# Kernel tuning notes

Hardware: AMD Instinct MI355X
Metric: run time of the kernel (lower is better)

The kernel has to match this reference:

```python
import jax, jax.numpy as jnp
import numpy as np

MIN_S = 0.05
MAX_S = 0.3
B, D = 16384, 2048
H = D // 4


def setup_inputs() -> dict:
    key = jax.random.key(0)
    k1, k2, k3 = jax.random.split(key, 3)
    x = jax.random.normal(k1, (B, D), dtype=jnp.float32)
    # sparsity predictor params (stored [in, out]); torch Linear default init scale
    s1 = 1.0 / np.sqrt(D)
    s2 = 1.0 / np.sqrt(H)
    W1 = jax.random.uniform(k2, (D, H), jnp.float32, -s1, s1)
    b1 = jnp.zeros((H,), jnp.float32)
    W2 = jax.random.uniform(k3, (H, 1), jnp.float32, -s2, s2)
    b2 = jnp.zeros((1,), jnp.float32)
    return {"x": x, "W1": W1, "b1": b1, "W2": W2, "b2": b2}


def reference(x, W1, b1, W2, b2):
    # sparsity predictor: Linear -> ReLU -> Linear -> Sigmoid, scaled to [min,max]
    h = jax.nn.relu(x @ W1 + b1)                         # [B, H]
    sig = jax.nn.sigmoid(h @ W2 + b2)                    # [B, 1]
    sparsity = MIN_S + (MAX_S - MIN_S) * sig             # [B, 1]

    d = x.shape[1]
    abs_x = jnp.abs(x)
    # per-row k = max(1, round(D * (1 - s))); torch uses Python round (half-even),
    # matching jnp.round semantics
    k = jnp.maximum(1, jnp.round(d * (1.0 - sparsity[:, 0])).astype(jnp.int32))  # [B]
    sorted_abs = jnp.sort(abs_x, axis=1)                 # [B, D] ascending
    threshold = jnp.take_along_axis(sorted_abs, (k - 1)[:, None], axis=1)        # [B, 1]

    mask = (abs_x > threshold).astype(x.dtype)           # [B, D]
    sparse_x = x * mask
    actual_sparsity = mask.sum(axis=1) / d               # [B]
    l1_reg = jnp.abs(sparse_x).sum(axis=1).mean()        # scalar
    return sparse_x, mask, sparsity, actual_sparsity, l1_reg
```

## Files before the change

kernel.cpp:

```cpp
#include <hip/hip_runtime.h>
#include <math.h>

#define B_ROWS 16384
#define D_DIM  2048
#define H_DIM  512

typedef __attribute__((ext_vector_type(8))) short  s16x8;
typedef __attribute__((ext_vector_type(4))) float  f32x4;

union U8 { unsigned short us[8]; s16x8 v; };
union U4 { unsigned short us[4]; short4 v; };

static __device__ __forceinline__ unsigned short f2bf(float f) {
    unsigned u = __float_as_uint(f);
    u += 0x7FFFu + ((u >> 16) & 1u);
    return (unsigned short)(u >> 16);
}

__global__ __launch_bounds__(256) void pack_w1(
    const float* __restrict__ W1, unsigned short* __restrict__ Wp)
{
    const int gid = blockIdx.x * 256 + threadIdx.x;
    const int ko = gid >> 9;
    const int n  = gid & 511;
    U8 h8, l8;
    #pragma unroll
    for (int j = 0; j < 8; ++j) {
        const float w = W1[(size_t)(ko * 8 + j) * H_DIM + n];
        const unsigned short h = f2bf(w);
        const float hf = __uint_as_float((unsigned)h << 16);
        h8.us[j] = h;
        l8.us[j] = f2bf(w - hf);
    }
    const int s    = ko >> 2;
    const int lane = (n & 15) | ((ko & 3) << 4);
    const int Nt   = n >> 4;
    const size_t baseH = ((((size_t)0 * 64 + s) * 32 + Nt) * 64 + lane) * 8;
    const size_t baseL = ((((size_t)1 * 64 + s) * 32 + Nt) * 64 + lane) * 8;
    *(s16x8*)(Wp + baseH) = h8.v;
    *(s16x8*)(Wp + baseL) = l8.v;
}

__global__ __launch_bounds__(512, 2) void predictor_gemm(
    const float* __restrict__ x, const unsigned short* __restrict__ Wp,
    const float* __restrict__ b1, const float* __restrict__ W2,
    double* __restrict__ logit)
{
    __shared__ __align__(16) unsigned short Abuf[2][2][2048];

    const int tid = threadIdx.x;
    const int l   = tid & 63;
    const int Nw  = tid >> 6;
    const int bx  = blockIdx.x;
    const int rowBase = bx * 64;
    const int NtBase  = Nw * 4;

    const int sm = tid >> 3;
    const int sh = tid & 7;
    const float* xp = x + (size_t)(rowBase + sm) * D_DIM + sh * 4;
    const int stIdx = (sm >> 4) * 512 + (((sm & 15) | ((sh >> 1) << 4)) << 3) + (sh & 1) * 4;
    unsigned short* stH[2] = {&Abuf[0][0][stIdx], &Abuf[1][0][stIdx]};
    unsigned short* stL[2] = {&Abuf[0][1][stIdx], &Abuf[1][1][stIdx]};

    const s16x8* WpV = (const s16x8*)Wp;

    f32x4 acc[4][4];
    #pragma unroll
    for (int mt = 0; mt < 4; ++mt)
        #pragma unroll
        for (int nt = 0; nt < 4; ++nt)
            acc[mt][nt] = {0.f, 0.f, 0.f, 0.f};

    {
        const float4 v = *(const float4*)(xp);
        const float xv[4] = {v.x, v.y, v.z, v.w};
        U4 h4, l4;
        #pragma unroll
        for (int j = 0; j < 4; ++j) {
            const unsigned short h = f2bf(xv[j]);
            h4.us[j] = h;
            l4.us[j] = f2bf(xv[j] - __uint_as_float((unsigned)h << 16));
        }
        *(short4*)stH[0] = h4.v;
        *(short4*)stL[0] = l4.v;
    }
    s16x8 Bh[4], Bl[4];
    #pragma unroll
    for (int nt = 0; nt < 4; ++nt) {
        Bh[nt] = WpV[((0 * 64 + 0) * 32 + NtBase + nt) * 64 + l];
        Bl[nt] = WpV[((1 * 64 + 0) * 32 + NtBase + nt) * 64 + l];
    }
    __syncthreads();

    for (int s = 0; s < 64; ++s) {
        const int cur = s & 1, nxt = cur ^ 1;
        s16x8 BhN[4], BlN[4];
        float4 xn;
        if (s < 63) {
            #pragma unroll
            for (int nt = 0; nt < 4; ++nt) {
                BhN[nt] = WpV[((0 * 64 + (s + 1)) * 32 + NtBase + nt) * 64 + l];
                BlN[nt] = WpV[((1 * 64 + (s + 1)) * 32 + NtBase + nt) * 64 + l];
            }
            xn = *(const float4*)(xp + (s + 1) * 32);
        }

        s16x8 Ah[4], Al[4];
        #pragma unroll
        for (int mt = 0; mt < 4; ++mt) {
            Ah[mt] = *(const s16x8*)&Abuf[cur][0][mt * 512 + l * 8];
            Al[mt] = *(const s16x8*)&Abuf[cur][1][mt * 512 + l * 8];
        }

        #pragma unroll
        for (int mt = 0; mt < 4; ++mt)
            #pragma unroll
            for (int nt = 0; nt < 4; ++nt) {
                acc[mt][nt] = __builtin_amdgcn_mfma_f32_16x16x32_bf16(Ah[mt], Bh[nt], acc[mt][nt], 0, 0, 0);
                acc[mt][nt] = __builtin_amdgcn_mfma_f32_16x16x32_bf16(Al[mt], Bh[nt], acc[mt][nt], 0, 0, 0);
                acc[mt][nt] = __builtin_amdgcn_mfma_f32_16x16x32_bf16(Ah[mt], Bl[nt], acc[mt][nt], 0, 0, 0);
            }

        if (s < 63) {
            const float xv[4] = {xn.x, xn.y, xn.z, xn.w};
            U4 h4, l4;
            #pragma unroll
            for (int j = 0; j < 4; ++j) {
                const unsigned short h = f2bf(xv[j]);
                h4.us[j] = h;
                l4.us[j] = f2bf(xv[j] - __uint_as_float((unsigned)h << 16));
            }
            *(short4*)stH[nxt] = h4.v;
            *(short4*)stL[nxt] = l4.v;
            #pragma unroll
            for (int nt = 0; nt < 4; ++nt) { Bh[nt] = BhN[nt]; Bl[nt] = BlN[nt]; }
        }
        __syncthreads();
    }

    float  b1v[4];
    double w2v[4];
    #pragma unroll
    for (int nt = 0; nt < 4; ++nt) {
        const int j = (NtBase + nt) * 16 + (l & 15);
        b1v[nt] = b1[j];
        w2v[nt] = (double)W2[j];
    }
    #pragma unroll
    for (int mt = 0; mt < 4; ++mt)
        #pragma unroll
        for (int reg = 0; reg < 4; ++reg) {
            double p = 0.0;
            #pragma unroll
            for (int nt = 0; nt < 4; ++nt) {
                const float h = acc[mt][nt][reg] + b1v[nt];
                if (h > 0.0f) p = fma((double)h, w2v[nt], p);
            }
            #pragma unroll
            for (int m2 = 1; m2 < 16; m2 <<= 1) p += __shfl_xor(p, m2, 64);
            if ((l & 15) == 0)
                atomicAdd(&logit[rowBase + mt * 16 + ((l >> 4) & 3) * 4 + reg], p);
        }
}

__global__ __launch_bounds__(256) void select_and_write(
    const float* __restrict__ x, const float* __restrict__ b2,
    const double* __restrict__ logit,
    float* __restrict__ out_sparse, float* __restrict__ out_mask,
    float* __restrict__ out_sparsity, float* __restrict__ out_actual,
    double* __restrict__ l1rows)
{
    __shared__ int hist[4][1024];

    const int tid = threadIdx.x;
    const int w = tid >> 6, l = tid & 63;
    const int row = blockIdx.x * 4 + w;
    int* hw = hist[w];

    const float4* x4 = (const float4*)(x + (size_t)row * D_DIM);
    float4 vv[8];
    #pragma unroll
    for (int i = 0; i < 8; ++i) vv[i] = x4[i * 64 + l];

    const double L = logit[row] + (double)b2[0];
    const double sig = 1.0 / (1.0 + exp(-L));
    const double s = 0.05 + 0.25 * sig;
    int k = (int)rint(2048.0 * (1.0 - s));
    if (k < 1) k = 1;
    if (k > 2048) k = 2048;
    if (l == 0) out_sparsity[row] = (float)s;

    int krem = k;
    unsigned prefix = 0;

    #pragma unroll
    for (int pass = 0; pass < 4; ++pass) {
        const int shift = 24 - pass * 8;
        const unsigned pmask = (pass == 0) ? 0u : (0xFFFFFFFFu << (shift + 8));

        #pragma unroll
        for (int j = 0; j < 4; ++j)
            ((int4*)hw)[l + 64 * j] = int4{0, 0, 0, 0};
        __builtin_amdgcn_wave_barrier();
        __threadfence_block();

        #pragma unroll
        for (int i = 0; i < 8; ++i) {
            const float qq[4] = {vv[i].x, vv[i].y, vv[i].z, vv[i].w};
            #pragma unroll
            for (int c = 0; c < 4; ++c) {
                const unsigned ub = __float_as_uint(qq[c]) & 0x7FFFFFFFu;
                if (pass == 0 || (ub & pmask) == prefix)
                    atomicAdd(&hw[((ub >> shift) & 255) * 4 + (l & 3)], 1);
            }
        }
        __builtin_amdgcn_wave_barrier();
        __threadfence_block();

        int b_[4], tot = 0;
        #pragma unroll
        for (int j = 0; j < 4; ++j) {
            const int4 c4 = ((const int4*)hw)[4 * l + j];
            b_[j] = c4.x + c4.y + c4.z + c4.w;
            tot += b_[j];
        }
        int sc = tot;
        #pragma unroll
        for (int off = 1; off < 64; off <<= 1) {
            const int n = __shfl_up(sc, off);
            if (l >= off) sc += n;
        }
        int cum = sc - tot;
        int found = 0;
        #pragma unroll
        for (int j = 0; j < 4; ++j) {
            if (krem > cum && krem <= cum + b_[j])
                found = ((4 * l + j) << 12) | (krem - cum);
            cum += b_[j];
        }
        #pragma unroll
        for (int m2 = 1; m2 < 64; m2 <<= 1) found |= __shfl_xor(found, m2);
        prefix |= ((unsigned)(found >> 12)) << shift;
        krem = found & 0xFFF;
    }
    const unsigned thr = prefix;

    float4* os4 = (float4*)(out_sparse + (size_t)row * D_DIM);
    float4* om4 = (float4*)(out_mask   + (size_t)row * D_DIM);
    int cnt = 0;
    double lp = 0.0;
    #pragma unroll
    for (int i = 0; i < 8; ++i) {
        const float qq[4] = {vv[i].x, vv[i].y, vv[i].z, vv[i].w};
        float sq[4], mq[4];
        #pragma unroll
        for (int c = 0; c < 4; ++c) {
            const unsigned ub = __float_as_uint(qq[c]) & 0x7FFFFFFFu;
            const bool keep = (ub > thr);
            mq[c] = keep ? 1.0f : 0.0f;
            sq[c] = keep ? qq[c] : 0.0f;
            cnt += keep ? 1 : 0;
            if (keep) lp += (double)fabsf(qq[c]);
        }
        os4[i * 64 + l] = float4{sq[0], sq[1], sq[2], sq[3]};
        om4[i * 64 + l] = float4{mq[0], mq[1], mq[2], mq[3]};
    }
    #pragma unroll
    for (int m2 = 1; m2 < 64; m2 <<= 1) {
        lp  += __shfl_xor(lp, m2);
        cnt += __shfl_xor(cnt, m2);
    }
    if (l == 0) {
        l1rows[row] = lp;
        out_actual[row] = (float)cnt * (1.0f / 2048.0f);
    }
}

__global__ __launch_bounds__(256) void finalize_l1(
    const double* __restrict__ l1rows, float* __restrict__ out_l1)
{
    __shared__ double sh[256];
    double s = 0.0;
    for (int i = threadIdx.x; i < B_ROWS; i += 256) s += l1rows[i];
    sh[threadIdx.x] = s;
    __syncthreads();
    for (int st = 128; st > 0; st >>= 1) {
        if (threadIdx.x < st) sh[threadIdx.x] += sh[threadIdx.x + st];
        __syncthreads();
    }
    if (threadIdx.x == 0) out_l1[0] = (float)(sh[0] / (double)B_ROWS);
}

extern "C" void kernel_launch(void* const* d_in, const int* in_sizes, int n_in,
                              void* d_out, int out_size, void* d_ws, size_t ws_size,
                              hipStream_t stream) {
    const float* x  = (const float*)d_in[0];
    const float* W1 = (const float*)d_in[1];
    const float* b1 = (const float*)d_in[2];
    const float* W2 = (const float*)d_in[3];
    const float* b2 = (const float*)d_in[4];

    float* out = (float*)d_out;
    float* out_sparse   = out;
    float* out_mask     = out + (size_t)B_ROWS * D_DIM;
    float* out_sparsity = out + 2ull * B_ROWS * D_DIM;
    float* out_actual   = out_sparsity + B_ROWS;
    float* out_l1       = out_actual + B_ROWS;

    double* logit  = (double*)d_ws;
    double* l1rows = logit + B_ROWS;
    unsigned short* Wp = (unsigned short*)(l1rows + B_ROWS);

    hipMemsetAsync(d_ws, 0, (size_t)B_ROWS * sizeof(double), stream);

    pack_w1<<<512, 256, 0, stream>>>(W1, Wp);
    predictor_gemm<<<B_ROWS / 64, 512, 0, stream>>>(x, Wp, b1, W2, logit);
    select_and_write<<<B_ROWS / 4, 256, 0, stream>>>(x, b2, logit, out_sparse, out_mask,
                                                     out_sparsity, out_actual, l1rows);
    finalize_l1<<<1, 256, 0, stream>>>(l1rows, out_l1);
}
```

Baseline: 505.7 us.

## Fuse predictor GEMM and top-k selection into one kernel per 64-row block

Merges the predictor GEMM and the per-row radix-select/write kernel into one kernel. Logits are reduced in shared memory instead of through global double atomics, which also removes the memset. The x rows are re-read right after the GEMM while they may still be cache resident, and the next row is prefetched while the current one is processed. The histogram is widened to 8 sub-bins per bucket to reduce LDS atomic contention. The select phase now runs on only 256 blocks of 8 waves each, with 8 rows per wave done serially, so it has less parallelism and latency hiding than the previous 4096-block launch.

Measured after the change: 534.5 us. 5.7% more time.

```diff
diff --git a/kernel.cpp b/kernel.cpp
--- a/kernel.cpp
+++ b/kernel.cpp
@@ -41,155 +41,11 @@
     *(s16x8*)(Wp + baseL) = l8.v;
 }
 
-__global__ __launch_bounds__(512, 2) void predictor_gemm(
-    const float* __restrict__ x, const unsigned short* __restrict__ Wp,
-    const float* __restrict__ b1, const float* __restrict__ W2,
-    double* __restrict__ logit)
+static __device__ __forceinline__ void process_row(
+    const float4 (&vv)[8], const size_t grow, const int k, const int l, int* hw,
+    float* __restrict__ out_sparse, float* __restrict__ out_mask,
+    float* __restrict__ out_actual, double* __restrict__ l1rows)
 {
-    __shared__ __align__(16) unsigned short Abuf[2][2][2048];
-
-    const int tid = threadIdx.x;
-    const int l   = tid & 63;
-    const int Nw  = tid >> 6;
-    const int bx  = blockIdx.x;
-    const int rowBase = bx * 64;
-    const int NtBase  = Nw * 4;
-
-    const int sm = tid >> 3;
-    const int sh = tid & 7;
-    const float* xp = x + (size_t)(rowBase + sm) * D_DIM + sh * 4;
-    const int stIdx = (sm >> 4) * 512 + (((sm & 15) | ((sh >> 1) << 4)) << 3) + (sh & 1) * 4;
-    unsigned short* stH[2] = {&Abuf[0][0][stIdx], &Abuf[1][0][stIdx]};
-    unsigned short* stL[2] = {&Abuf[0][1][stIdx], &Abuf[1][1][stIdx]};
-
-    const s16x8* WpV = (const s16x8*)Wp;
-
-    f32x4 acc[4][4];
-    #pragma unroll
-    for (int mt = 0; mt < 4; ++mt)
-        #pragma unroll
-        for (int nt = 0; nt < 4; ++nt)
-            acc[mt][nt] = {0.f, 0.f, 0.f, 0.f};
-
-    {
-        const float4 v = *(const float4*)(xp);
-        const float xv[4] = {v.x, v.y, v.z, v.w};
-        U4 h4, l4;
-        #pragma unroll
-        for (int j = 0; j < 4; ++j) {
-            const unsigned short h = f2bf(xv[j]);
-            h4.us[j] = h;
-            l4.us[j] = f2bf(xv[j] - __uint_as_float((unsigned)h << 16));
-        }
-        *(short4*)stH[0] = h4.v;
-        *(short4*)stL[0] = l4.v;
-    }
-    s16x8 Bh[4], Bl[4];
-    #pragma unroll
-    for (int nt = 0; nt < 4; ++nt) {
-        Bh[nt] = WpV[((0 * 64 + 0) * 32 + NtBase + nt) * 64 + l];
-        Bl[nt] = WpV[((1 * 64 + 0) * 32 + NtBase + nt) * 64 + l];
-    }
-    __syncthreads();
-
-    for (int s = 0; s < 64; ++s) {
-        const int cur = s & 1, nxt = cur ^ 1;
-        s16x8 BhN[4], BlN[4];
-        float4 xn;
-        if (s < 63) {
-            #pragma unroll
-            for (int nt = 0; nt < 4; ++nt) {
-                BhN[nt] = WpV[((0 * 64 + (s + 1)) * 32 + NtBase + nt) * 64 + l];
-                BlN[nt] = WpV[((1 * 64 + (s + 1)) * 32 + NtBase + nt) * 64 + l];
-            }
-            xn = *(const float4*)(xp + (s + 1) * 32);
-        }
-
-        s16x8 Ah[4], Al[4];
-        #pragma unroll
-        for (int mt = 0; mt < 4; ++mt) {
-            Ah[mt] = *(const s16x8*)&Abuf[cur][0][mt * 512 + l * 8];
-            Al[mt] = *(const s16x8*)&Abuf[cur][1][mt * 512 + l * 8];
-        }
-
-        #pragma unroll
-        for (int mt = 0; mt < 4; ++mt)
-            #pragma unroll
-            for (int nt = 0; nt < 4; ++nt) {
-                acc[mt][nt] = __builtin_amdgcn_mfma_f32_16x16x32_bf16(Ah[mt], Bh[nt], acc[mt][nt], 0, 0, 0);
-                acc[mt][nt] = __builtin_amdgcn_mfma_f32_16x16x32_bf16(Al[mt], Bh[nt], acc[mt][nt], 0, 0, 0);
-                acc[mt][nt] = __builtin_amdgcn_mfma_f32_16x16x32_bf16(Ah[mt], Bl[nt], acc[mt][nt], 0, 0, 0);
-            }
-
-        if (s < 63) {
-            const float xv[4] = {xn.x, xn.y, xn.z, xn.w};
-            U4 h4, l4;
-            #pragma unroll
-            for (int j = 0; j < 4; ++j) {
-                const unsigned short h = f2bf(xv[j]);
-                h4.us[j] = h;
-                l4.us[j] = f2bf(xv[j] - __uint_as_float((unsigned)h << 16));
-            }
-            *(short4*)stH[nxt] = h4.v;
-            *(short4*)stL[nxt] = l4.v;
-            #pragma unroll
-            for (int nt = 0; nt < 4; ++nt) { Bh[nt] = BhN[nt]; Bl[nt] = BlN[nt]; }
-        }
-        __syncthreads();
-    }
-
-    float  b1v[4];
-    double w2v[4];
-    #pragma unroll
-    for (int nt = 0; nt < 4; ++nt) {
-        const int j = (NtBase + nt) * 16 + (l & 15);
-        b1v[nt] = b1[j];
-        w2v[nt] = (double)W2[j];
-    }
-    #pragma unroll
-    for (int mt = 0; mt < 4; ++mt)
-        #pragma unroll
-        for (int reg = 0; reg < 4; ++reg) {
-            double p = 0.0;
-            #pragma unroll
-            for (int nt = 0; nt < 4; ++nt) {
-                const float h = acc[mt][nt][reg] + b1v[nt];
-                if (h > 0.0f) p = fma((double)h, w2v[nt], p);
-            }
-            #pragma unroll
-            for (int m2 = 1; m2 < 16; m2 <<= 1) p += __shfl_xor(p, m2, 64);
-            if ((l & 15) == 0)
-                atomicAdd(&logit[rowBase + mt * 16 + ((l >> 4) & 3) * 4 + reg], p);
-        }
-}
-
-__global__ __launch_bounds__(256) void select_and_write(
-    const float* __restrict__ x, const float* __restrict__ b2,
-    const double* __restrict__ logit,
-    float* __restrict__ out_sparse, float* __restrict__ out_mask,
-    float* __restrict__ out_sparsity, float* __restrict__ out_actual,
-    double* __restrict__ l1rows)
-{
-    __shared__ int hist[4][1024];
-
-    const int tid = threadIdx.x;
-    const int w = tid >> 6, l = tid & 63;
-    const int row = blockIdx.x * 4 + w;
-    int* hw = hist[w];
-
-    const float4* x4 = (const float4*)(x + (size_t)row * D_DIM);
-    float4 vv[8];
-    #pragma unroll
-    for (int i = 0; i < 8; ++i) vv[i] = x4[i * 64 + l];
-
-    const double L = logit[row] + (double)b2[0];
-    const double sig = 1.0 / (1.0 + exp(-L));
-    const double s = 0.05 + 0.25 * sig;
-    int k = (int)rint(2048.0 * (1.0 - s));
-    if (k < 1) k = 1;
-    if (k > 2048) k = 2048;
-    if (l == 0) out_sparsity[row] = (float)s;
-
     int krem = k;
     unsigned prefix = 0;
 
@@ -199,7 +55,7 @@
         const unsigned pmask = (pass == 0) ? 0u : (0xFFFFFFFFu << (shift + 8));
 
         #pragma unroll
-        for (int j = 0; j < 4; ++j)
+        for (int j = 0; j < 8; ++j)
             ((int4*)hw)[l + 64 * j] = int4{0, 0, 0, 0};
         __builtin_amdgcn_wave_barrier();
         __threadfence_block();
@@ -211,7 +67,7 @@
             for (int c = 0; c < 4; ++c) {
                 const unsigned ub = __float_as_uint(qq[c]) & 0x7FFFFFFFu;
                 if (pass == 0 || (ub & pmask) == prefix)
-                    atomicAdd(&hw[((ub >> shift) & 255) * 4 + (l & 3)], 1);
+                    atomicAdd(&hw[((ub >> shift) & 255) * 8 + (l & 7)], 1);
             }
         }
         __builtin_amdgcn_wave_barrier();
@@ -220,8 +76,9 @@
         int b_[4], tot = 0;
         #pragma unroll
         for (int j = 0; j < 4; ++j) {
-            const int4 c4 = ((const int4*)hw)[4 * l + j];
-            b_[j] = c4.x + c4.y + c4.z + c4.w;
+            const int4 c0 = ((const int4*)hw)[(4 * l + j) * 2 + 0];
+            const int4 c1 = ((const int4*)hw)[(4 * l + j) * 2 + 1];
+            b_[j] = c0.x + c0.y + c0.z + c0.w + c1.x + c1.y + c1.z + c1.w;
             tot += b_[j];
         }
         int sc = tot;
@@ -245,8 +102,8 @@
     }
     const unsigned thr = prefix;
 
-    float4* os4 = (float4*)(out_sparse + (size_t)row * D_DIM);
-    float4* om4 = (float4*)(out_mask   + (size_t)row * D_DIM);
+    float4* os4 = (float4*)(out_sparse + grow * D_DIM);
+    float4* om4 = (float4*)(out_mask   + grow * D_DIM);
     int cnt = 0;
     double lp = 0.0;
     #pragma unroll
@@ -271,8 +128,180 @@
         cnt += __shfl_xor(cnt, m2);
     }
     if (l == 0) {
-        l1rows[row] = lp;
-        out_actual[row] = (float)cnt * (1.0f / 2048.0f);
+        l1rows[grow] = lp;
+        out_actual[grow] = (float)cnt * (1.0f / 2048.0f);
+    }
+}
+
+__global__ __launch_bounds__(512, 2) void fused_main(
+    const float* __restrict__ x, const unsigned short* __restrict__ Wp,
+    const float* __restrict__ b1, const float* __restrict__ W2,
+    const float* __restrict__ b2,
+    float* __restrict__ out_sparse, float* __restrict__ out_mask,
+    float* __restrict__ out_sparsity, float* __restrict__ out_actual,
+    double* __restrict__ l1rows)
+{
+    __shared__ __align__(16) union {
+        struct {
+            unsigned short Abuf[2][2][2048];
+            double partials[8][64];
+        } p1;
+        int hist[8][2048];
+    } sh;
+    __shared__ int kLDS[64];
+
+    const int tid = threadIdx.x;
+    const int l   = tid & 63;
+    const int Nw  = tid >> 6;
+    const int bx  = blockIdx.x;
+    const int rowBase = bx * 64;
+    const int NtBase  = Nw * 4;
+
+    const int sm = tid >> 3;
+    const int shh = tid & 7;
+    const float* xp = x + (size_t)(rowBase + sm) * D_DIM + shh * 4;
+    const int stIdx = (sm >> 4) * 512 + (((sm & 15) | ((shh >> 1) << 4)) << 3) + (shh & 1) * 4;
+    unsigned short* stH[2] = {&sh.p1.Abuf[0][0][stIdx], &sh.p1.Abuf[1][0][stIdx]};
+    unsigned short* stL[2] = {&sh.p1.Abuf[0][1][stIdx], &sh.p1.Abuf[1][1][stIdx]};
+
+    const s16x8* WpV = (const s16x8*)Wp;
+
+    f32x4 acc[4][4];
+    #pragma unroll
+    for (int mt = 0; mt < 4; ++mt)
+        #pragma unroll
+        for (int nt = 0; nt < 4; ++nt)
+            acc[mt][nt] = {0.f, 0.f, 0.f, 0.f};
+
+    {
+        const float4 v = *(const float4*)(xp);
+        const float xv[4] = {v.x, v.y, v.z, v.w};
+        U4 h4, l4;
+        #pragma unroll
+        for (int j = 0; j < 4; ++j) {
+            const unsigned short h = f2bf(xv[j]);
+            h4.us[j] = h;
+            l4.us[j] = f2bf(xv[j] - __uint_as_float((unsigned)h << 16));
+        }
+        *(short4*)stH[0] = h4.v;
+        *(short4*)stL[0] = l4.v;
+    }
+    s16x8 Bh[4], Bl[4];
+    #pragma unroll
+    for (int nt = 0; nt < 4; ++nt) {
+        Bh[nt] = WpV[((0 * 64 + 0) * 32 + NtBase + nt) * 64 + l];
+        Bl[nt] = WpV[((1 * 64 + 0) * 32 + NtBase + nt) * 64 + l];
+    }
+    __syncthreads();
+
+    for (int s = 0; s < 64; ++s) {
+        const int cur = s & 1, nxt = cur ^ 1;
+        s16x8 BhN[4], BlN[4];
+        float4 xn;
+        if (s < 63) {
+            #pragma unroll
+            for (int nt = 0; nt < 4; ++nt) {
+                BhN[nt] = WpV[((0 * 64 + (s + 1)) * 32 + NtBase + nt) * 64 + l];
+                BlN[nt] = WpV[((1 * 64 + (s + 1)) * 32 + NtBase + nt) * 64 + l];
+            }
+            xn = *(const float4*)(xp + (s + 1) * 32);
+        }
+
+        s16x8 Ah[4], Al[4];
+        #pragma unroll
+        for (int mt = 0; mt < 4; ++mt) {
+            Ah[mt] = *(const s16x8*)&sh.p1.Abuf[cur][0][mt * 512 + l * 8];
+            Al[mt] = *(const s16x8*)&sh.p1.Abuf[cur][1][mt * 512 + l * 8];
+        }
+
+        #pragma unroll
+        for (int mt = 0; mt < 4; ++mt)
+            #pragma unroll
+            for (int nt = 0; nt < 4; ++nt) {
+                acc[mt][nt] = __builtin_amdgcn_mfma_f32_16x16x32_bf16(Ah[mt], Bh[nt], acc[mt][nt], 0, 0, 0);
+                acc[mt][nt] = __builtin_amdgcn_mfma_f32_16x16x32_bf16(Al[mt], Bh[nt], acc[mt][nt], 0, 0, 0);
+                acc[mt][nt] = __builtin_amdgcn_mfma_f32_16x16x32_bf16(Ah[mt], Bl[nt], acc[mt][nt], 0, 0, 0);
+            }
+
+        if (s < 63) {
+            const float xv[4] = {xn.x, xn.y, xn.z, xn.w};
+            U4 h4, l4;
+            #pragma unroll
+            for (int j = 0; j < 4; ++j) {
+                const unsigned short h = f2bf(xv[j]);
+                h4.us[j] = h;
+                l4.us[j] = f2bf(xv[j] - __uint_as_float((unsigned)h << 16));
+            }
+            *(short4*)stH[nxt] = h4.v;
+            *(short4*)stL[nxt] = l4.v;
+            #pragma unroll
+            for (int nt = 0; nt < 4; ++nt) { Bh[nt] = BhN[nt]; Bl[nt] = BlN[nt]; }
+        }
+        __syncthreads();
+    }
+
+    {
+        float  b1v[4];
+        double w2v[4];
+        #pragma unroll
+        for (int nt = 0; nt < 4; ++nt) {
+            const int j = (NtBase + nt) * 16 + (l & 15);
+            b1v[nt] = b1[j];
+            w2v[nt] = (double)W2[j];
+        }
+        #pragma unroll
+        for (int mt = 0; mt < 4; ++mt)
+            #pragma unroll
+            for (int reg = 0; reg < 4; ++reg) {
+                double p = 0.0;
+                #pragma unroll
+                for (int nt = 0; nt < 4; ++nt) {
+                    const float h = acc[mt][nt][reg] + b1v[nt];
+                    if (h > 0.0f) p = fma((double)h, w2v[nt], p);
+                }
+                #pragma unroll
+                for (int m2 = 1; m2 < 16; m2 <<= 1) p += __shfl_xor(p, m2, 64);
+                if ((l & 15) == 0)
+                    sh.p1.partials[Nw][mt * 16 + ((l >> 4) & 3) * 4 + reg] = p;
+            }
+    }
+    __syncthreads();
+
+    if (tid < 64) {
+        double L = (double)b2[0];
+        #pragma unroll
+        for (int w = 0; w < 8; ++w) L += sh.p1.partials[w][tid];
+        const double sig = 1.0 / (1.0 + exp(-L));
+        const double sv = 0.05 + 0.25 * sig;
+        int k = (int)rint(2048.0 * (1.0 - sv));
+        if (k < 1) k = 1;
+        if (k > 2048) k = 2048;
+        kLDS[tid] = k;
+        out_sparsity[rowBase + tid] = (float)sv;
+    }
+    __syncthreads();
+
+    int* hw = sh.hist[Nw];
+    const size_t growBase = (size_t)rowBase + Nw * 8;
+    const float4* xb = (const float4*)x + growBase * (D_DIM / 4);
+
+    float4 vvA[8], vvB[8];
+    #pragma unroll
+    for (int i = 0; i < 8; ++i) vvA[i] = xb[i * 64 + l];
+
+    #pragma unroll
+    for (int rp = 0; rp < 4; ++rp) {
+        const int rA = 2 * rp, rB = 2 * rp + 1;
+        #pragma unroll
+        for (int i = 0; i < 8; ++i) vvB[i] = xb[(size_t)rB * 512 + i * 64 + l];
+        process_row(vvA, growBase + rA, kLDS[Nw * 8 + rA], l, hw,
+                    out_sparse, out_mask, out_actual, l1rows);
+        if (rp < 3) {
+            #pragma unroll
+            for (int i = 0; i < 8; ++i) vvA[i] = xb[(size_t)(rB + 1) * 512 + i * 64 + l];
+        }
+        process_row(vvB, growBase + rB, kLDS[Nw * 8 + rB], l, hw,
+                    out_sparse, out_mask, out_actual, l1rows);
     }
 }
 
@@ -307,15 +336,12 @@
     float* out_actual   = out_sparsity + B_ROWS;
     float* out_l1       = out_actual + B_ROWS;
 
-    double* logit  = (double*)d_ws;
-    double* l1rows = logit + B_ROWS;
+    double* l1rows = (double*)d_ws;
     unsigned short* Wp = (unsigned short*)(l1rows + B_ROWS);
 
-    hipMemsetAsync(d_ws, 0, (size_t)B_ROWS * sizeof(double), stream);
-
     pack_w1<<<512, 256, 0, stream>>>(W1, Wp);
-    predictor_gemm<<<B_ROWS / 64, 512, 0, stream>>>(x, Wp, b1, W2, logit);
-    select_and_write<<<B_ROWS / 4, 256, 0, stream>>>(x, b2, logit, out_sparse, out_mask,
-                                                     out_sparsity, out_actual, l1rows);
+    fused_main<<<B_ROWS / 64, 512, 0, stream>>>(x, Wp, b1, W2, b2,
+                                                out_sparse, out_mask, out_sparsity,
+                                                out_actual, l1rows);
     finalize_l1<<<1, 256, 0, stream>>>(l1rows, out_l1);
 }
```
